# Optimization experiments

Hardware: AMD Instinct MI355X
Metric: run time of the kernel (lower is better)

Reference implementation:

```python
import jax, jax.numpy as jnp
import numpy as np
from jax import lax


def _conv(x, w, b=None):
    # NCHW conv, 'same' padding, stride 1
    y = lax.conv_general_dilated(x, w, (1, 1), 'SAME',
                                 dimension_numbers=('NCHW', 'OIHW', 'NCHW'))
    return y if b is None else y + b[None, :, None, None]


def _up2(x):
    # nn.Upsample(scale_factor=2), nearest
    return jnp.repeat(jnp.repeat(x, 2, axis=2), 2, axis=3)


def _rot_attn(x, wq, wk, wv, lng, lnb, reach=1):
    # Batched sliding-window rotatory cross-attention (replaces the Python loop
    # over window positions).  x: [B, C, H, W]; each position i in [reach, B-reach)
    # attends (as query) to its 2*reach neighbor frames.
    B, C, H, W = x.shape
    xs = x.reshape(B, C, H * W).transpose(0, 2, 1)          # [B, N, C]
    tgt = xs[reach:B - reach]                               # [P, N, C]
    offs = [o for o in range(-reach, reach + 1) if o != 0]  # fixed small set
    nbs = jnp.stack([xs[reach + o: B - reach + o] for o in offs], axis=1)  # [P,2r,N,C]
    q = tgt @ wq
    k = nbs @ wk
    v = nbs @ wv
    scores = jnp.einsum('pnc,pjmc->pjnm', q, k) / jnp.asarray(C, x.dtype) ** 0.5
    ctx = jnp.einsum('pjnm,pjmc->pjnc', jax.nn.softmax(scores, axis=-1), v).mean(1)  # [P,N,C]
    # LayerNorm over C
    mu = ctx.mean(-1, keepdims=True)
    var = ((ctx - mu) ** 2).mean(-1, keepdims=True)
    ctx = (ctx - mu) * lax.rsqrt(var + 1e-5) * lng + lnb
    cm = ctx.mean(0)                                        # mean over positions [N,C]
    return x + cm.T.reshape(C, H, W)[None]                  # broadcast residual


def _block(h, skip, w_up, b_up, wq, wk, wv, lng, lnb, bng, bnb, w_cb):
    h = _conv(_up2(h), w_up, b_up)                          # 1x1 conv
    h = jnp.concatenate([h, skip], axis=1)
    h = _rot_attn(h, wq, wk, wv, lng, lnb)
    # ConvolutionBatchNormblock: BN (batch stats, eps=1e-5) -> ReLU -> conv (no bias)
    mu = h.mean((0, 2, 3))
    var = ((h - mu[None, :, None, None]) ** 2).mean((0, 2, 3))
    h = (h - mu[None, :, None, None]) * lax.rsqrt(var + 1e-5)[None, :, None, None]
    h = h * bng[None, :, None, None] + bnb[None, :, None, None]
    return _conv(jax.nn.relu(h), w_cb)


def setup_inputs() -> dict:
    key = jax.random.key(0)
    ks = iter(jax.random.split(key, 64))
    n = lambda shape, s: jax.random.normal(next(ks), shape, jnp.float32) * s
    d = {}
    d['x'] = n([6, 64, 768], 1.0)
    d['skip0'] = n([6, 256, 16, 16], 1.0)
    d['skip1'] = n([6, 128, 32, 32], 1.0)
    d['skip2'] = n([6, 64, 64, 64], 1.0)
    d['w_sc'] = n([512, 768, 3, 3], 0.02)
    d['b_sc'] = jnp.zeros([512], jnp.float32)
    for i, (cin, cout) in enumerate([(512, 256), (256, 128), (128, 64)], 1):
        s = cin ** -0.5
        d[f'w_up{i}'] = n([cout, cin, 1, 1], s)
        d[f'b_up{i}'] = jnp.zeros([cout], jnp.float32)
        d[f'wq{i}'] = n([cin, cin], s)
        d[f'wk{i}'] = n([cin, cin], s)
        d[f'wv{i}'] = n([cin, cin], s)
        d[f'lng{i}'] = jnp.ones([cin], jnp.float32)
        d[f'lnb{i}'] = jnp.zeros([cin], jnp.float32)
        d[f'bng{i}'] = jnp.ones([cin], jnp.float32)
        d[f'bnb{i}'] = jnp.zeros([cin], jnp.float32)
        d[f'w_cb{i}'] = n([cout, cin, 3, 3], s * 0.3)
    return d


def reference(x, skip0, skip1, skip2, w_sc, b_sc,
              w_up1, b_up1, wq1, wk1, wv1, lng1, lnb1, bng1, bnb1, w_cb1,
              w_up2, b_up2, wq2, wk2, wv2, lng2, lnb2, bng2, bnb2, w_cb2,
              w_up3, b_up3, wq3, wk3, wv3, lng3, lnb3, bng3, bnb3, w_cb3):
    B, N, D = x.shape
    g = int(N ** 0.5)  # 8x8 token grid (image_size*2 / patch_size)
    h = _conv(x.transpose(0, 2, 1).reshape(B, D, g, g), w_sc, b_sc)   # [B,512,8,8]
    h = _block(h, skip0, w_up1, b_up1, wq1, wk1, wv1, lng1, lnb1, bng1, bnb1, w_cb1)
    h = _block(h, skip1, w_up2, b_up2, wq2, wk2, wv2, lng2, lnb2, bng2, bnb2, w_cb2)
    h = _block(h, skip2, w_up3, b_up3, wq3, wk3, wv3, lng3, lnb3, bng3, bnb3, w_cb3)
    return _up2(h)                                                    # [B,64,128,128]
```

## Files before the change

### kernel.cpp

```cpp
#include <hip/hip_runtime.h>
#include <hip/hip_bf16.h>

typedef const float* fp;
typedef unsigned short u16;
typedef __attribute__((ext_vector_type(8))) short short8v;
typedef __attribute__((ext_vector_type(4))) float f32x4;

__device__ __forceinline__ u16 f2b(float f){
  union{float f; unsigned u;} x; x.f = f;
  unsigned r = x.u + 0x7FFFu + ((x.u>>16)&1u);
  return (u16)(r>>16);
}

__global__ __launch_bounds__(256) void k_fill(float* out, int n, float v){
  int i = blockIdx.x*256 + threadIdx.x;
  if(i < n) out[i] = v;
}
__global__ __launch_bounds__(256) void k_fillb(float* out, fp bias, int Cout, int N){
  int i = blockIdx.x*256 + threadIdx.x;
  if(i < 6*Cout*N) out[i] = bias[(i/N)%Cout];
}
__global__ __launch_bounds__(256) void k_b16(fp in, u16* o, int n){
  int i = (blockIdx.x*256 + threadIdx.x)*8;
  if(i >= n) return;
  u16 tmp[8];
  #pragma unroll
  for(int e=0;e<8;e++) tmp[e] = f2b(in[i+e]);
  *(short8v*)(o+i) = *(const short8v*)tmp;
}
__global__ __launch_bounds__(256) void k_wtr(fp w, u16* wt, int Cout, int Cin){
  int idx = blockIdx.x*256 + threadIdx.x;
  int cc = Cout*Cin;
  if(idx >= 9*cc) return;
  int tap = idx / cc, rem = idx - tap*cc;
  wt[idx] = f2b(w[(size_t)rem*9 + tap]);
}
__global__ __launch_bounds__(256) void k_wqkvt(fp wq, fp wk, fp wv, u16* bt, int C, float rs){
  int idx = blockIdx.x*256 + threadIdx.x;
  if(idx >= 3*C*C) return;
  int r = idx / C, ci = idx - r*C;
  int sel = r / C, co = r - sel*C;
  float v = (sel==0 ? wq : sel==1 ? wk : wv)[(size_t)ci*C + co];
  bt[idx] = f2b(sel==0 ? v*rs : v);
}

__global__ __launch_bounds__(256) void k_in_tr(fp x, float* h0){
  int n = blockIdx.x, b = blockIdx.y;
  for(int d = threadIdx.x; d < 768; d += blockDim.x)
    h0[((size_t)b*768 + d)*64 + n] = x[((size_t)b*64 + n)*768 + d];
}

__global__ __launch_bounds__(256) void k_conv3_mfma2(const u16* __restrict__ wt,
    const u16* __restrict__ inb16, float* __restrict__ out,
    int Cin, int Cout, int H, int W, int S){
  const int N = H*W;
  __shared__ u16 As[64*40];
  __shared__ u16 Bs[64*40];
  int t = threadIdx.x, wid = t>>6, lane = t&63, l15 = lane&15, g = lane>>4;
  int b = blockIdx.z / S, s = blockIdx.z % S;
  int co0 = blockIdx.y*64, px0 = blockIdx.x*64;
  int ciN = Cin/S, ci0 = s*ciN;
  const u16* inb = inb16 + (size_t)b*Cin*N;
  int arow = t>>2, acol = (t&3)*8;
  int bpx = t&63, boct = t>>6;
  int p = px0 + bpx, py = p/W, px_ = p - py*W;
  int nc = ciN >> 5, nk = 9*nc;
  f32x4 acc[4];
  #pragma unroll
  for(int i=0;i<4;i++) acc[i] = f32x4{0.f,0.f,0.f,0.f};
  short8v av; u16 bt[8];

  #define PREF(ks) { int tap = (ks)/nc; int c0 = ((ks) - tap*nc)<<5;                     \
      int dy = tap/3 - 1, dx = tap - (tap/3)*3 - 1;                                      \
      av = *(const short8v*)(wt + ((size_t)tap*Cout + co0 + arow)*Cin + ci0 + c0 + acol);\
      bool val = ((unsigned)(py+dy) < (unsigned)H) && ((unsigned)(px_+dx) < (unsigned)W);\
      const u16* bp = inb + (size_t)(ci0 + c0 + boct*8)*N + (p + dy*W + dx);             \
      _Pragma("unroll") for(int e=0;e<8;e++) bt[e] = val ? bp[(size_t)e*N] : (u16)0; }

  PREF(0);
  for(int ks = 0; ks < nk; ks++){
    __syncthreads();
    *(short8v*)(As + arow*40 + acol) = av;
    *(short8v*)(Bs + bpx*40 + boct*8) = *(const short8v*)bt;
    __syncthreads();
    if(ks+1 < nk) PREF(ks+1);
    short8v a = *(const short8v*)(As + (wid*16+l15)*40 + 8*g);
    #pragma unroll
    for(int pt=0; pt<4; pt++){
      short8v bf = *(const short8v*)(Bs + (pt*16+l15)*40 + 8*g);
      acc[pt] = __builtin_amdgcn_mfma_f32_16x16x32_bf16(a, bf, acc[pt], 0,0,0);
    }
  }
  #undef PREF
  #pragma unroll
  for(int pt=0; pt<4; pt++){
    #pragma unroll
    for(int r=0; r<4; r++){
      size_t o = ((size_t)b*Cout + co0 + wid*16 + 4*g + r)*N + px0 + pt*16 + l15;
      if(S == 1) out[o] = acc[pt][r];
      else atomicAdd(out + o, acc[pt][r]);
    }
  }
}

__global__ __launch_bounds__(256) void k_gemm_qkv(const u16* __restrict__ XB,
    const u16* __restrict__ BT, u16* __restrict__ Qo, u16* __restrict__ Ko,
    u16* __restrict__ Vo, int C, int Nn){
  __shared__ u16 As[64*40], Bs[64*40];
  int t = threadIdx.x, wid = t>>6, lane = t&63, l15 = lane&15, g = lane>>4;
  int r0 = blockIdx.x*64, c0 = blockIdx.y*64;
  int arow = t>>2, acol = (t&3)*8;
  int nk = C/32;
  f32x4 acc[4];
  #pragma unroll
  for(int i=0;i<4;i++) acc[i] = f32x4{0.f,0.f,0.f,0.f};
  short8v av = *(const short8v*)(XB + (size_t)(r0+arow)*C + acol);
  short8v bv = *(const short8v*)(BT + (size_t)(c0+arow)*C + acol);
  for(int ks = 0; ks < nk; ks++){
    __syncthreads();
    *(short8v*)(As + arow*40 + acol) = av;
    *(short8v*)(Bs + arow*40 + acol) = bv;
    __syncthreads();
    if(ks+1 < nk){
      int k0 = (ks+1)*32;
      av = *(const short8v*)(XB + (size_t)(r0+arow)*C + k0 + acol);
      bv = *(const short8v*)(BT + (size_t)(c0+arow)*C + k0 + acol);
    }
    short8v a = *(const short8v*)(As + (wid*16+l15)*40 + 8*g);
    #pragma unroll
    for(int pt=0; pt<4; pt++){
      short8v bf = *(const short8v*)(Bs + (pt*16+l15)*40 + 8*g);
      acc[pt] = __builtin_amdgcn_mfma_f32_16x16x32_bf16(a, bf, acc[pt], 0,0,0);
    }
  }
  int sel = c0 / C, cb = c0 - sel*C;
  if(sel < 2){
    u16* ob = sel==0 ? Qo : Ko;
    #pragma unroll
    for(int pt=0; pt<4; pt++){
      #pragma unroll
      for(int r=0; r<4; r++)
        ob[(size_t)(r0 + wid*16 + 4*g + r)*C + cb + pt*16 + l15] = f2b(acc[pt][r]);
    }
  }else{
    int b = r0 / Nn, nb = r0 - b*Nn;
    #pragma unroll
    for(int pt=0; pt<4; pt++){
      #pragma unroll
      for(int r=0; r<4; r++)
        Vo[((size_t)b*C + cb + pt*16 + l15)*Nn + nb + wid*16 + 4*g + r] = f2b(acc[pt][r]);
    }
  }
}

__global__ void k_conv1_low(const float* __restrict__ in, fp w, fp bias,
                            float* __restrict__ out, int Cin, int Cout, int N1){
  int bc = blockIdx.x; int b = bc / Cout; int co = bc % Cout;
  extern __shared__ float ws[];
  for(int i = threadIdx.x; i < Cin; i += blockDim.x) ws[i] = w[(size_t)co*Cin + i];
  __syncthreads();
  const float* inb = in + (size_t)b*Cin*N1;
  float bv = bias[co];
  for(int p = threadIdx.x; p < N1; p += blockDim.x){
    float acc = bv;
    for(int ci = 0; ci < Cin; ci++) acc += inb[(size_t)ci*N1 + p] * ws[ci];
    out[((size_t)b*Cout + co)*N1 + p] = acc;
  }
}

__global__ __launch_bounds__(256) void k_concat_up(const float* __restrict__ a, fp skip,
                                                   float* __restrict__ cat,
                                                   int Ca, int Cs, int N2, int W2){
  int bc = blockIdx.x; int C = Ca + Cs; int b = bc / C; int c = bc % C;
  float* o = cat + (size_t)bc*N2;
  if(c < Ca){
    const float* s = a + ((size_t)b*Ca + c)*(N2/4);
    int W1 = W2/2;
    for(int n = threadIdx.x; n < N2; n += blockDim.x){
      int y = n / W2, x = n % W2;
      o[n] = s[(y>>1)*W1 + (x>>1)];
    }
  }else{
    fp s = skip + ((size_t)b*Cs + (c-Ca))*N2;
    for(int n = threadIdx.x; n < N2; n += blockDim.x) o[n] = s[n];
  }
}

__global__ __launch_bounds__(256) void k_trb(const float* __restrict__ src, u16* __restrict__ dst,
                                             int C, int N){
  __shared__ float tb[32][33];
  int b = blockIdx.z;
  int c0 = blockIdx.y*32, n0 = blockIdx.x*32;
  int tx = threadIdx.x & 31, ty = threadIdx.x >> 5;
  for(int i = ty; i < 32; i += 8) tb[i][tx] = src[((size_t)b*C + c0+i)*N + n0+tx];
  __syncthreads();
  for(int i = ty; i < 32; i += 8) dst[((size_t)b*N + n0+i)*C + c0+tx] = f2b(tb[tx][i]);
}

__global__ __launch_bounds__(256) void k_attn128(const u16* __restrict__ Q,
                                                 const u16* __restrict__ K,
                                                 const u16* __restrict__ VT,
                                                 float* __restrict__ ctxn, int N){
  constexpr int C = 128, KVB = 64, KP = C+8, VP = KVB+8, PSP = 68;
  __shared__ u16 Ks[KVB*KP];
  __shared__ u16 Vt[C*VP];
  __shared__ u16 ps[4][16*PSP];
  int t = threadIdx.x, wid = t>>6, lane = t&63, l15 = lane&15, g = lane>>4;
  int p = blockIdx.y, q0 = (blockIdx.x*4 + wid)*16, j = blockIdx.z;
  const u16* Qb = Q + ((size_t)(p+1)*N + q0)*C;
  const u16* Kb = K  + (size_t)(p + (j?2:0))*N*C;
  const u16* Vb = VT + (size_t)(p + (j?2:0))*C*N;
  short8v qf[4];
  #pragma unroll
  for(int kk = 0; kk < 4; kk++)
    qf[kk] = *(const short8v*)(Qb + (size_t)l15*C + kk*32 + 8*g);
  f32x4 acc[8];
  #pragma unroll
  for(int i=0;i<8;i++) acc[i] = f32x4{0.f,0.f,0.f,0.f};
  float m[4] = {-1e30f,-1e30f,-1e30f,-1e30f};
  float l[4] = {0.f,0.f,0.f,0.f};
  short8v kpre[4], vpre[4];

  #define APREF(M0) { _Pragma("unroll") for(int i=0;i<4;i++){                  \
        int idx = t*8 + i*2048; int mm = idx>>7, cc = idx&127;                 \
        kpre[i] = *(const short8v*)(Kb + (size_t)((M0)+mm)*C + cc); }          \
      _Pragma("unroll") for(int i=0;i<4;i++){                                  \
        int idx = t*8 + i*2048; int c = idx>>6, mo = idx&63;                   \
        vpre[i] = *(const short8v*)(Vb + (size_t)c*N + (M0) + mo); } }

  APREF(0);
  for(int m0 = 0; m0 < N; m0 += KVB){
    __syncthreads();
    #pragma unroll
    for(int i=0;i<4;i++){ int idx = t*8 + i*2048; int mm = idx>>7, cc = idx&127;
      *(short8v*)(Ks + mm*KP + cc) = kpre[i]; }
    #pragma unroll
    for(int i=0;i<4;i++){ int idx = t*8 + i*2048; int c = idx>>6, mo = idx&63;
      *(short8v*)(Vt + c*VP + mo) = vpre[i]; }
    __syncthreads();
    if(m0 + KVB < N) APREF(m0 + KVB);
    f32x4 s[4];
    __builtin_amdgcn_s_setprio(1);
    #pragma unroll
    for(int h=0; h<4; h++){
      s[h] = f32x4{0.f,0.f,0.f,0.f};
      #pragma unroll
      for(int kk=0; kk<4; kk++){
        short8v kf = *(const short8v*)(Ks + (h*16+l15)*KP + kk*32 + 8*g);
        s[h] = __builtin_amdgcn_mfma_f32_16x16x32_bf16(qf[kk], kf, s[h], 0,0,0);
      }
    }
    __builtin_amdgcn_s_setprio(0);
    float lmax[4]; bool need = false;
    #pragma unroll
    for(int r=0; r<4; r++){
      float a = fmaxf(fmaxf(s[0][r],s[1][r]), fmaxf(s[2][r],s[3][r]));
      lmax[r] = a; need |= (a > m[r] + 8.f);
    }
    if(__any((int)need)){
      #pragma unroll
      for(int r=0; r<4; r++){
        float mx = lmax[r];
        #pragma unroll
        for(int off=1; off<16; off<<=1) mx = fmaxf(mx, __shfl_xor(mx, off));
        float mnew = fmaxf(m[r], mx);
        float scl = __expf(m[r] - mnew);
        l[r] *= scl; m[r] = mnew;
        #pragma unroll
        for(int ct=0; ct<8; ct++) acc[ct][r] *= scl;
      }
    }
    #pragma unroll
    for(int r=0; r<4; r++){
      float ls = 0.f;
      #pragma unroll
      for(int h=0; h<4; h++){
        float e = __expf(s[h][r] - m[r]); ls += e;
        ps[wid][(4*g+r)*PSP + h*16 + l15] = f2b(e);
      }
      l[r] += ls;
    }
    __builtin_amdgcn_s_setprio(1);
    #pragma unroll
    for(int ks=0; ks<2; ks++){
      short8v pa = *(const short8v*)(ps[wid] + l15*PSP + ks*32 + 8*g);
      #pragma unroll
      for(int ct=0; ct<8; ct++){
        short8v vb = *(const short8v*)(Vt + (ct*16+l15)*VP + ks*32 + 8*g);
        acc[ct] = __builtin_amdgcn_mfma_f32_16x16x32_bf16(pa, vb, acc[ct], 0,0,0);
      }
    }
    __builtin_amdgcn_s_setprio(0);
  }
  #undef APREF
  float inv[4];
  #pragma unroll
  for(int r=0; r<4; r++){
    float lr = l[r];
    #pragma unroll
    for(int off=1; off<16; off<<=1) lr += __shfl_xor(lr, off);
    inv[r] = 0.5f/lr;
  }
  #pragma unroll
  for(int ct=0; ct<8; ct++){
    int c = ct*16 + l15;
    #pragma unroll
    for(int r=0; r<4; r++)
      atomicAdd(&ctxn[((size_t)p*N + q0 + 4*g + r)*C + c], acc[ct][r]*inv[r]);
  }
}

template<int C>
__global__ __launch_bounds__(256) void k_attn_mfma(const u16* __restrict__ Q,
                                                   const u16* __restrict__ K,
                                                   const u16* __restrict__ VT,
                                                   float* __restrict__ ctxn, int N){
  constexpr int KP = C + 8;
  __shared__ u16 Ks[32*KP];
  __shared__ u16 Vt[C*40];
  __shared__ u16 ps[4][16*40];
  int t = threadIdx.x, wid = t>>6, lane = t&63;
  int l15 = lane&15, g = lane>>4;
  int p = blockIdx.y, j = blockIdx.z;
  int q0 = (blockIdx.x*4 + wid)*16;
  const u16* Qb = Q + ((size_t)(p+1)*N + q0)*C;
  const u16* Kb = K  + (size_t)(p + (j?2:0))*N*C;
  const u16* Vb = VT + (size_t)(p + (j?2:0))*C*N;

  short8v qf[C/32];
  #pragma unroll
  for(int kk = 0; kk < C/32; kk++)
    qf[kk] = *(const short8v*)(Qb + (size_t)l15*C + kk*32 + 8*g);

  f32x4 acc[C/16];
  #pragma unroll
  for(int i = 0; i < C/16; i++) acc[i] = f32x4{0.f,0.f,0.f,0.f};
  float mrow[4] = {-1e30f,-1e30f,-1e30f,-1e30f};
  float lrow[4] = {0.f,0.f,0.f,0.f};

  for(int m0 = 0; m0 < N; m0 += 32){
    __syncthreads();
    for(int idx = t*8; idx < 32*C; idx += 2048){
      int m = idx/C, c = idx - m*C;
      *(short8v*)(Ks + m*KP + c) = *(const short8v*)(Kb + (size_t)(m0+m)*C + c);
    }
    for(int idx = t*8; idx < 32*C; idx += 2048){
      int c = idx >> 5, mo = idx & 31;
      *(short8v*)(Vt + c*40 + mo) = *(const short8v*)(Vb + (size_t)c*N + m0 + mo);
    }
    __syncthreads();
    f32x4 s0 = {0.f,0.f,0.f,0.f}, s1 = {0.f,0.f,0.f,0.f};
    #pragma unroll
    for(int kk = 0; kk < C/32; kk++){
      short8v k0 = *(const short8v*)(Ks + l15*KP      + kk*32 + 8*g);
      short8v k1 = *(const short8v*)(Ks + (16+l15)*KP + kk*32 + 8*g);
      s0 = __builtin_amdgcn_mfma_f32_16x16x32_bf16(qf[kk], k0, s0, 0,0,0);
      s1 = __builtin_amdgcn_mfma_f32_16x16x32_bf16(qf[kk], k1, s1, 0,0,0);
    }
    float scl[4];
    #pragma unroll
    for(int r = 0; r < 4; r++){
      float mx = fmaxf(s0[r], s1[r]);
      #pragma unroll
      for(int off = 1; off < 16; off <<= 1) mx = fmaxf(mx, __shfl_xor(mx, off));
      float mnew = fmaxf(mrow[r], mx);
      scl[r] = __expf(mrow[r] - mnew);
      float e0 = __expf(s0[r] - mnew), e1 = __expf(s1[r] - mnew);
      float psum = e0 + e1;
      #pragma unroll
      for(int off = 1; off < 16; off <<= 1) psum += __shfl_xor(psum, off);
      lrow[r] = lrow[r]*scl[r] + psum;
      mrow[r] = mnew;
      int m = 4*g + r;
      ps[wid][m*40 + l15]      = f2b(e0);
      ps[wid][m*40 + 16 + l15] = f2b(e1);
    }
    #pragma unroll
    for(int ct = 0; ct < C/16; ct++){
      #pragma unroll
      for(int r = 0; r < 4; r++) acc[ct][r] *= scl[r];
    }
    short8v pa = *(const short8v*)(ps[wid] + l15*40 + 8*g);
    #pragma unroll
    for(int ct = 0; ct < C/16; ct++){
      short8v vb = *(const short8v*)(Vt + (ct*16+l15)*40 + 8*g);
      acc[ct] = __builtin_amdgcn_mfma_f32_16x16x32_bf16(pa, vb, acc[ct], 0,0,0);
    }
  }
  #pragma unroll
  for(int ct = 0; ct < C/16; ct++){
    int c = ct*16 + l15;
    #pragma unroll
    for(int r = 0; r < 4; r++){
      int m = 4*g + r;
      atomicAdd(&ctxn[((size_t)p*N + q0 + m)*C + c], 0.5f*acc[ct][r]/lrow[r]);
    }
  }
}

__global__ __launch_bounds__(64) void k_ln64(float* __restrict__ ctxn, fp lng, fp lnb, int C){
  float* row = ctxn + (size_t)blockIdx.x*C;
  int t = threadIdx.x;
  float s = 0.f, s2 = 0.f;
  for(int c = t; c < C; c += 64){ float v = row[c]; s += v; s2 += v*v; }
  #pragma unroll
  for(int off = 32; off > 0; off >>= 1){ s += __shfl_xor(s, off); s2 += __shfl_xor(s2, off); }
  float m = s/(float)C, var = s2/(float)C - m*m;
  float ri = rsqrtf(var + 1e-5f);
  for(int c = t; c < C; c += 64) row[c] = (row[c] - m)*ri*lng[c] + lnb[c];
}

__global__ void k_cm(const float* __restrict__ ctxn, float* __restrict__ cm, int C, int N){
  int n = blockIdx.x;
  for(int c = threadIdx.x; c < C; c += blockDim.x){
    float s = 0.25f*( ctxn[((size_t)0*N + n)*C + c] + ctxn[((size_t)1*N + n)*C + c]
                    + ctxn[((size_t)2*N + n)*C + c] + ctxn[((size_t)3*N + n)*C + c]);
    cm[(size_t)n*C + c] = s;
  }
}

__global__ __launch_bounds__(256) void k_addstat(float* __restrict__ h, const float* __restrict__ cm,
                                                 float* __restrict__ ss2, int C, int N){
  int bc = blockIdx.x; int c = bc % C;
  float* hp = h + (size_t)bc*N;
  float s = 0.f, s2 = 0.f;
  for(int n = threadIdx.x; n < N; n += blockDim.x){
    float v = hp[n] + cm[(size_t)n*C + c];
    hp[n] = v; s += v; s2 += v*v;
  }
  #pragma unroll
  for(int o = 32; o > 0; o >>= 1){ s += __shfl_down(s, o); s2 += __shfl_down(s2, o); }
  if((threadIdx.x & 63) == 0){
    atomicAdd(&ss2[c], s); atomicAdd(&ss2[C + c], s2);
  }
}
__global__ void k_bnfin(const float* __restrict__ ss2, fp bng, fp bnb,
                        float* __restrict__ ss, int C, int N){
  int c = threadIdx.x;
  if(c >= C) return;
  float inv = 1.f/(6.f*(float)N);
  float m = ss2[c]*inv, var = ss2[C+c]*inv - m*m;
  float sc = bng[c]*rsqrtf(var + 1e-5f);
  ss[c] = sc; ss[C + c] = bnb[c] - m*sc;
}

__global__ __launch_bounds__(256) void k_bnrelu2(float* __restrict__ h, const float* __restrict__ ssin,
                                                 u16* __restrict__ ob, int C, int N){
  int bc = blockIdx.x; int c = bc % C;
  float sc = ssin[c], sh = ssin[C + c];
  float* hp = h + (size_t)bc*N;
  u16* op = ob + (size_t)bc*N;
  for(int n = threadIdx.x; n < N; n += blockDim.x){
    float v = hp[n]*sc + sh; v = v > 0.f ? v : 0.f;
    hp[n] = v; op[n] = f2b(v);
  }
}

__global__ __launch_bounds__(256) void k_up_out(const float* __restrict__ in, float* out,
                                                int H, int W){
  int bc = blockIdx.x;
  const float* ip = in + (size_t)bc*H*W;
  float* op = out + (size_t)bc*4*H*W;
  int W2 = 2*W, N2 = 4*H*W;
  for(int p = threadIdx.x; p < N2; p += blockDim.x){
    int y = p / W2, x = p % W2;
    op[p] = ip[(y>>1)*W + (x>>1)];
  }
}

extern "C" void kernel_launch(void* const* d_in, const int* in_sizes, int n_in,
                              void* d_out, int out_size, void* d_ws, size_t ws_size,
                              hipStream_t stream){
  float* out_f = (float*)d_out;
  static const int EXP[36] = {294912,393216,786432,1572864,3538944,512,
    131072,256,262144,262144,262144,512,512,512,512,1179648,
    32768,128,65536,65536,65536,256,256,256,256,294912,
    8192,64,16384,16384,16384,128,128,128,128,73728};
  bool ok = (n_in == 36) && (out_size == 6291456);
  if(ok) for(int i = 0; i < 36; i++) if(in_sizes[i] != EXP[i]){ ok = false; break; }
  if(!ok){
    k_fill<<<(out_size+255)/256, 256, 0, stream>>>(out_f, out_size, 10.0f);
    return;
  }
  const size_t R = 3145728;
  const size_t NEED = (5*R + 4096)*sizeof(float);
  if(ws_size < NEED){
    k_fill<<<(out_size+255)/256, 256, 0, stream>>>(out_f, out_size, 100.0f);
    return;
  }
  (void)hipGetLastError();
  #define CKERR(code) do{ if(hipGetLastError() != hipSuccess){ \
      k_fill<<<(out_size+255)/256, 256, 0, stream>>>(out_f, out_size, (float)(code)); \
      return; } }while(0)

  fp x = (fp)d_in[0];
  fp skip[3]  = {(fp)d_in[1],(fp)d_in[2],(fp)d_in[3]};
  fp w_sc = (fp)d_in[4], b_sc = (fp)d_in[5];
  fp w_up[3] = {(fp)d_in[6], (fp)d_in[16],(fp)d_in[26]};
  fp b_up[3] = {(fp)d_in[7], (fp)d_in[17],(fp)d_in[27]};
  fp wq[3]   = {(fp)d_in[8], (fp)d_in[18],(fp)d_in[28]};
  fp wk[3]   = {(fp)d_in[9], (fp)d_in[19],(fp)d_in[29]};
  fp wv[3]   = {(fp)d_in[10],(fp)d_in[20],(fp)d_in[30]};
  fp lng[3]  = {(fp)d_in[11],(fp)d_in[21],(fp)d_in[31]};
  fp lnb[3]  = {(fp)d_in[12],(fp)d_in[22],(fp)d_in[32]};
  fp bng[3]  = {(fp)d_in[13],(fp)d_in[23],(fp)d_in[33]};
  fp bnb[3]  = {(fp)d_in[14],(fp)d_in[24],(fp)d_in[34]};
  fp w_cb[3] = {(fp)d_in[15],(fp)d_in[25],(fp)d_in[35]};

  float* Wp = (float*)d_ws;
  float *Cc = Wp, *CT = Wp + R;
  u16 *QB = (u16*)(Wp + 2*R), *KB = (u16*)(Wp + 3*R), *VB = (u16*)(Wp + 4*R);
  float *SS  = Wp + 5*R;
  float *SS2 = Wp + 5*R + 2048;
  float *OB = Wp + R, *Bf = Wp + 2*R, *CM = Wp + 2*R;
  u16 *XB  = QB + R;
  u16 *WQT = KB + R;
  u16 *WT = KB, *IB = VB;

  k_in_tr<<<dim3(64,6),256,0,stream>>>(x, Cc);
  k_b16<<<(294912/8+255)/256, 256, 0, stream>>>(Cc, IB, 294912);
  k_wtr<<<(9*512*768+255)/256, 256, 0, stream>>>(w_sc, WT, 512, 768);
  k_fillb<<<(6*512*64+255)/256, 256, 0, stream>>>(OB, b_sc, 512, 64);
  k_conv3_mfma2<<<dim3(1,8,6*8), 256, 0, stream>>>(WT, IB, OB, 768, 512, 8, 8, 8);
  CKERR(20);

  const int Cskip[3] = {256,128,64};
  const int Hs[3]    = {16,32,64};
  const int SPL[3]   = {4,2,1};
  int Cprev = 512;
  for(int i = 0; i < 3; i++){
    int H = Hs[i], N = H*H;
    int N1 = N/4;
    int Cup = Cprev/2;
    int C = Cup + Cskip[i];
    k_conv1_low<<<6*Cup, (N1<256?N1:256), Cprev*4, stream>>>(OB, w_up[i], b_up[i], Bf, Cprev, Cup, N1);
    k_concat_up<<<6*C, 256, 0, stream>>>(Bf, skip[i], Cc, Cup, Cskip[i], N, H);
    k_trb<<<dim3(N/32, C/32, 6), 256, 0, stream>>>(Cc, XB, C, N);
    float rsv = 1.f/sqrtf((float)C);
    k_wqkvt<<<(3*C*C+255)/256, 256, 0, stream>>>(wq[i], wk[i], wv[i], WQT, C, rsv);
    k_gemm_qkv<<<dim3(6*N/64, 3*C/64), 256, 0, stream>>>(XB, WQT, QB, KB, VB, C, N);
    CKERR(30 + 10*i);
    k_fill<<<(4*N*C+255)/256, 256, 0, stream>>>(CT, 4*N*C, 0.f);
    if(i==0) k_attn_mfma<512><<<dim3(N/64,4,2),256,0,stream>>>(QB,KB,VB,CT,N);
    if(i==1) k_attn_mfma<256><<<dim3(N/64,4,2),256,0,stream>>>(QB,KB,VB,CT,N);
    if(i==2) k_attn128<<<dim3(N/64,4,2),256,0,stream>>>(QB,KB,VB,CT,N);
    k_ln64<<<4*N, 64, 0, stream>>>(CT, lng[i], lnb[i], C);
    CKERR(32 + 10*i);
    k_cm<<<N, C, 0, stream>>>(CT, CM, C, N);
    k_fill<<<(2*C+255)/256, 256, 0, stream>>>(SS2, 2*C, 0.f);
    k_addstat<<<6*C, 256, 0, stream>>>(Cc, CM, SS2, C, N);
    k_bnfin<<<1, C, 0, stream>>>(SS2, bng[i], bnb[i], SS, C, N);
    k_bnrelu2<<<6*C, 256, 0, stream>>>(Cc, SS, IB, C, N);
    int Co = C/2, S = SPL[i];
    k_wtr<<<(9*Co*C+255)/256, 256, 0, stream>>>(w_cb[i], WT, Co, C);
    if(S > 1) k_fill<<<(6*Co*N+255)/256, 256, 0, stream>>>(OB, 6*Co*N, 0.f);
    k_conv3_mfma2<<<dim3(N/64, Co/64, 6*S), 256, 0, stream>>>(WT, IB, OB, C, Co, H, H, S);
    CKERR(34 + 10*i);
    Cprev = Co;
  }
  k_up_out<<<6*64, 256, 0, stream>>>(OB, out_f, 64, 64);
  CKERR(90);
  #undef CKERR
}
```

Baseline: 751.4 us.

## Split attention KV range across wave pairs with in-block softmax merge

Replaces the C=128 attention kernel and the C=256 instantiation with a templated kernel in which each pair of waves shares a 16-query tile and splits the key range in half. Each wave keeps its own running max and sum, and the two halves are merged through shared memory before the atomic accumulation. The grid doubles so that more blocks are in flight for the smaller stages. For C=256, V is read straight from global memory rather than staged in LDS, which saves shared memory but may add global-load latency; the merge step adds extra synchronisation.

Result: no change. 758.7 us (+1.0%).

```diff
diff --git a/kernel.cpp b/kernel.cpp
--- a/kernel.cpp
+++ b/kernel.cpp
@@ -197,56 +197,67 @@
   for(int i = ty; i < 32; i += 8) dst[((size_t)b*N + n0+i)*C + c0+tx] = f2b(tb[tx][i]);
 }
 
-__global__ __launch_bounds__(256) void k_attn128(const u16* __restrict__ Q,
-                                                 const u16* __restrict__ K,
-                                                 const u16* __restrict__ VT,
-                                                 float* __restrict__ ctxn, int N){
-  constexpr int C = 128, KVB = 64, KP = C+8, VP = KVB+8, PSP = 68;
-  __shared__ u16 Ks[KVB*KP];
-  __shared__ u16 Vt[C*VP];
+template<int C, bool VL>
+__global__ __launch_bounds__(256) void k_attn_sp(const u16* __restrict__ Q,
+    const u16* __restrict__ K, const u16* __restrict__ VT,
+    float* __restrict__ ctxn, int N){
+  constexpr int KVB = 32, KP = C+8, VP = 40, PSP = 40, NP = C/32, CP4 = C+4;
+  __shared__ u16 Ks[2*KVB*KP];
+  __shared__ u16 Vt[VL ? 2*C*VP : 8];
   __shared__ u16 ps[4][16*PSP];
   int t = threadIdx.x, wid = t>>6, lane = t&63, l15 = lane&15, g = lane>>4;
-  int p = blockIdx.y, q0 = (blockIdx.x*4 + wid)*16, j = blockIdx.z;
+  int half = wid & 1, qgrp = wid >> 1;
+  int lt = ((t>>7)<<6) | (t&63);
+  int p = blockIdx.y, j = blockIdx.z;
+  int q0 = (blockIdx.x*2 + qgrp)*16;
   const u16* Qb = Q + ((size_t)(p+1)*N + q0)*C;
   const u16* Kb = K  + (size_t)(p + (j?2:0))*N*C;
   const u16* Vb = VT + (size_t)(p + (j?2:0))*C*N;
-  short8v qf[4];
-  #pragma unroll
-  for(int kk = 0; kk < 4; kk++)
+  u16* Ksh = Ks + half*(KVB*KP);
+  u16* Vth = Vt + (VL ? half*(C*VP) : 0);
+  int kbase = half*(N>>1);
+
+  short8v qf[NP];
+  #pragma unroll
+  for(int kk=0;kk<NP;kk++)
     qf[kk] = *(const short8v*)(Qb + (size_t)l15*C + kk*32 + 8*g);
-  f32x4 acc[8];
-  #pragma unroll
-  for(int i=0;i<8;i++) acc[i] = f32x4{0.f,0.f,0.f,0.f};
+  f32x4 acc[C/16];
+  #pragma unroll
+  for(int i=0;i<C/16;i++) acc[i] = f32x4{0.f,0.f,0.f,0.f};
   float m[4] = {-1e30f,-1e30f,-1e30f,-1e30f};
   float l[4] = {0.f,0.f,0.f,0.f};
-  short8v kpre[4], vpre[4];
-
-  #define APREF(M0) { _Pragma("unroll") for(int i=0;i<4;i++){                  \
-        int idx = t*8 + i*2048; int mm = idx>>7, cc = idx&127;                 \
-        kpre[i] = *(const short8v*)(Kb + (size_t)((M0)+mm)*C + cc); }          \
-      _Pragma("unroll") for(int i=0;i<4;i++){                                  \
-        int idx = t*8 + i*2048; int c = idx>>6, mo = idx&63;                   \
-        vpre[i] = *(const short8v*)(Vb + (size_t)c*N + (M0) + mo); } }
-
-  APREF(0);
-  for(int m0 = 0; m0 < N; m0 += KVB){
-    __syncthreads();
-    #pragma unroll
-    for(int i=0;i<4;i++){ int idx = t*8 + i*2048; int mm = idx>>7, cc = idx&127;
-      *(short8v*)(Ks + mm*KP + cc) = kpre[i]; }
-    #pragma unroll
-    for(int i=0;i<4;i++){ int idx = t*8 + i*2048; int c = idx>>6, mo = idx&63;
-      *(short8v*)(Vt + c*VP + mo) = vpre[i]; }
-    __syncthreads();
-    if(m0 + KVB < N) APREF(m0 + KVB);
-    f32x4 s[4];
+  short8v kpre[NP], vpre[NP];
+
+  #define APREF(M0) { _Pragma("unroll") for(int i_=0;i_<NP;i_++){                 \
+        int idx = lt*8 + i_*1024; int mm = idx/C, cc = idx - mm*C;                \
+        kpre[i_] = *(const short8v*)(Kb + (size_t)((M0)+mm)*C + cc); }            \
+      if constexpr(VL){ _Pragma("unroll") for(int i_=0;i_<NP;i_++){               \
+        int idx = lt*8 + i_*1024; int c = idx>>5, mo = idx&31;                    \
+        vpre[i_] = *(const short8v*)(Vb + (size_t)c*N + (M0) + mo); } } }
+
+  const int nit = N>>6;
+  APREF(kbase);
+  for(int it = 0; it < nit; ++it){
+    int m0 = kbase + it*KVB;
+    __syncthreads();
+    #pragma unroll
+    for(int i_=0;i_<NP;i_++){ int idx = lt*8 + i_*1024; int mm = idx/C, cc = idx - mm*C;
+      *(short8v*)(Ksh + mm*KP + cc) = kpre[i_]; }
+    if constexpr(VL){
+      #pragma unroll
+      for(int i_=0;i_<NP;i_++){ int idx = lt*8 + i_*1024; int c = idx>>5, mo = idx&31;
+        *(short8v*)(Vth + c*VP + mo) = vpre[i_]; }
+    }
+    __syncthreads();
+    if(it+1 < nit) APREF(kbase + (it+1)*KVB);
+    f32x4 s[2];
     __builtin_amdgcn_s_setprio(1);
     #pragma unroll
-    for(int h=0; h<4; h++){
+    for(int h=0; h<2; h++){
       s[h] = f32x4{0.f,0.f,0.f,0.f};
       #pragma unroll
-      for(int kk=0; kk<4; kk++){
-        short8v kf = *(const short8v*)(Ks + (h*16+l15)*KP + kk*32 + 8*g);
+      for(int kk=0; kk<NP; kk++){
+        short8v kf = *(const short8v*)(Ksh + (h*16+l15)*KP + kk*32 + 8*g);
         s[h] = __builtin_amdgcn_mfma_f32_16x16x32_bf16(qf[kk], kf, s[h], 0,0,0);
       }
     }
@@ -254,7 +265,7 @@
     float lmax[4]; bool need = false;
     #pragma unroll
     for(int r=0; r<4; r++){
-      float a = fmaxf(fmaxf(s[0][r],s[1][r]), fmaxf(s[2][r],s[3][r]));
+      float a = fmaxf(s[0][r], s[1][r]);
       lmax[r] = a; need |= (a > m[r] + 8.f);
     }
     if(__any((int)need)){
@@ -267,46 +278,77 @@
         float scl = __expf(m[r] - mnew);
         l[r] *= scl; m[r] = mnew;
         #pragma unroll
-        for(int ct=0; ct<8; ct++) acc[ct][r] *= scl;
+        for(int ct=0; ct<C/16; ct++) acc[ct][r] *= scl;
       }
     }
     #pragma unroll
     for(int r=0; r<4; r++){
       float ls = 0.f;
       #pragma unroll
-      for(int h=0; h<4; h++){
+      for(int h=0; h<2; h++){
         float e = __expf(s[h][r] - m[r]); ls += e;
         ps[wid][(4*g+r)*PSP + h*16 + l15] = f2b(e);
       }
       l[r] += ls;
     }
     __builtin_amdgcn_s_setprio(1);
-    #pragma unroll
-    for(int ks=0; ks<2; ks++){
-      short8v pa = *(const short8v*)(ps[wid] + l15*PSP + ks*32 + 8*g);
-      #pragma unroll
-      for(int ct=0; ct<8; ct++){
-        short8v vb = *(const short8v*)(Vt + (ct*16+l15)*VP + ks*32 + 8*g);
-        acc[ct] = __builtin_amdgcn_mfma_f32_16x16x32_bf16(pa, vb, acc[ct], 0,0,0);
-      }
+    short8v pa = *(const short8v*)(ps[wid] + l15*PSP + 8*g);
+    #pragma unroll
+    for(int ct=0; ct<C/16; ct++){
+      short8v vb;
+      if constexpr(VL) vb = *(const short8v*)(Vth + (ct*16+l15)*VP + 8*g);
+      else             vb = *(const short8v*)(Vb + (size_t)(ct*16+l15)*N + m0 + 8*g);
+      acc[ct] = __builtin_amdgcn_mfma_f32_16x16x32_bf16(pa, vb, acc[ct], 0,0,0);
     }
     __builtin_amdgcn_s_setprio(0);
   }
   #undef APREF
-  float inv[4];
   #pragma unroll
   for(int r=0; r<4; r++){
     float lr = l[r];
     #pragma unroll
     for(int off=1; off<16; off<<=1) lr += __shfl_xor(lr, off);
-    inv[r] = 0.5f/lr;
-  }
-  #pragma unroll
-  for(int ct=0; ct<8; ct++){
-    int c = ct*16 + l15;
-    #pragma unroll
-    for(int r=0; r<4; r++)
-      atomicAdd(&ctxn[((size_t)p*N + q0 + 4*g + r)*C + c], acc[ct][r]*inv[r]);
+    l[r] = lr;
+  }
+  float* accb = (float*)Ks;
+  float* mlb  = (float*)ps;
+  __syncthreads();
+  if(half == 1){
+    #pragma unroll
+    for(int ct=0; ct<C/16; ct++){
+      #pragma unroll
+      for(int r=0; r<4; r++)
+        accb[(size_t)(qgrp*16 + 4*g + r)*CP4 + ct*16 + l15] = acc[ct][r];
+    }
+    if(l15 == 0){
+      #pragma unroll
+      for(int r=0; r<4; r++){
+        mlb[(qgrp*16 + 4*g + r)*2]     = m[r];
+        mlb[(qgrp*16 + 4*g + r)*2 + 1] = l[r];
+      }
+    }
+  }
+  __syncthreads();
+  if(half == 0){
+    float fa[4], fb[4], inv[4];
+    #pragma unroll
+    for(int r=0; r<4; r++){
+      int row = qgrp*16 + 4*g + r;
+      float mb = mlb[row*2], lb = mlb[row*2 + 1];
+      float ms = fmaxf(m[r], mb);
+      fa[r] = __expf(m[r] - ms); fb[r] = __expf(mb - ms);
+      inv[r] = 0.5f/(l[r]*fa[r] + lb*fb[r]);
+    }
+    #pragma unroll
+    for(int ct=0; ct<C/16; ct++){
+      int c = ct*16 + l15;
+      #pragma unroll
+      for(int r=0; r<4; r++){
+        int row = qgrp*16 + 4*g + r;
+        float o = acc[ct][r]*fa[r] + accb[(size_t)row*CP4 + c]*fb[r];
+        atomicAdd(&ctxn[((size_t)p*N + q0 + 4*g + r)*C + c], o*inv[r]);
+      }
+    }
   }
 }
 
@@ -542,8 +584,8 @@
     CKERR(30 + 10*i);
     k_fill<<<(4*N*C+255)/256, 256, 0, stream>>>(CT, 4*N*C, 0.f);
     if(i==0) k_attn_mfma<512><<<dim3(N/64,4,2),256,0,stream>>>(QB,KB,VB,CT,N);
-    if(i==1) k_attn_mfma<256><<<dim3(N/64,4,2),256,0,stream>>>(QB,KB,VB,CT,N);
-    if(i==2) k_attn128<<<dim3(N/64,4,2),256,0,stream>>>(QB,KB,VB,CT,N);
+    if(i==1) k_attn_sp<256,false><<<dim3(N/32,4,2),256,0,stream>>>(QB,KB,VB,CT,N);
+    if(i==2) k_attn_sp<128,true ><<<dim3(N/32,4,2),256,0,stream>>>(QB,KB,VB,CT,N);
     k_ln64<<<4*N, 64, 0, stream>>>(CT, lng[i], lnb[i], C);
     CKERR(32 + 10*i);
     k_cm<<<N, C, 0, stream>>>(CT, CM, C, N);
```
